# Optimization experiments

Measured on AMD Instinct MI355X. Metric: run time of the kernel, lower is better.

The kernel has to match this reference:

```python
import jax, jax.numpy as jnp
import numpy as np

NEG_INF = -jnp.inf


def _forward(q, k, v, q_indexer, k_indexer, weights, index_topk, end_pos):
    b, h, s, d = q.shape
    scale = float(1.0 / np.sqrt(d))

    # ---- bf16_index: per-head relu(qk) weighted-sum over indexer heads ----
    qi = jnp.swapaxes(q_indexer, 1, 2).astype(jnp.float32)        # [b,hi,s,di]
    ki = jnp.transpose(k_indexer, (0, 2, 3, 1)).astype(jnp.float32)  # [b,hk,di,s] (hk=1 broadcasts)
    p = jax.nn.relu(jnp.matmul(qi, ki))                            # [b,hi,s,s]
    index_score = jnp.einsum('bhqk,bqh->bqk', p, weights.astype(jnp.float32))  # [b,s,s]

    # ---- causal additive mask (attn_mask=None path) ----
    causal = jnp.where(jnp.triu(jnp.ones((s, s), bool), 1), NEG_INF, 0.0).astype(jnp.float32)
    index_score = index_score + causal[None]

    # ---- top-k sparse index selection ----
    K = min(int(index_topk), int(end_pos))
    topk_score, topk_idx = jax.lax.top_k(index_score, K)           # [b,s,K]
    qpos = jnp.arange(s)[None, :, None]
    valid = topk_idx <= qpos
    # invalid slots: torch writes -1 (wraps to last col on CUDA); last col is causally
    # masked for those rows, so dropping the scatter gives an identical final mask.
    scatter_idx = jnp.where(valid, topk_idx, s)
    index_mask = jnp.full((b, s, s), NEG_INF).at[
        jnp.arange(b)[:, None, None], jnp.arange(s)[None, :, None], scatter_idx
    ].set(0.0, mode='drop')

    am = causal[None] + index_mask                                 # [b,s,s]
    masked = jnp.isinf(am) & (am < 0)                              # True = masked out
    keep = ~masked[:, None]                                        # [b,1,s,s]

    # ---- sparse SDPA ----
    scores = jnp.einsum('bhqd,bhkd->bhqk', q, k) * scale
    scores = jnp.where(keep, scores, NEG_INF)
    attn = jax.nn.softmax(scores.astype(jnp.float32), axis=-1)     # [b,h,s,s]
    output = jnp.einsum('bhqk,bhkd->bhqd', attn.astype(q.dtype), v)

    # ---- indexer auxiliary loss (main attn dist uses detached q,k) ----
    main_attn_dist = jax.lax.stop_gradient(attn).sum(axis=1)       # [b,s,s]
    gather_idx = jnp.where(valid, topk_idx, s - 1)                 # -1 wraps to last col
    sel = jnp.take_along_axis(main_attn_dist, gather_idx, axis=-1) # [b,s,K]
    pdist = jax.nn.softmax(topk_score.astype(jnp.float32), axis=-1)
    tgt = sel / jnp.maximum(jnp.sum(jnp.abs(sel), axis=-1, keepdims=True), 1e-12)
    # F.kl_div(log(p+eps), tgt+eps): t*(log t - log p)
    kl = (tgt + 1e-8) * (jnp.log(tgt + 1e-8) - jnp.log(pdist + 1e-8))
    loss = kl.sum(-1).mean()
    return loss, output


def setup_inputs() -> dict:
    key = jax.random.key(0)
    ks = jax.random.split(key, 6)
    b, h, s, d = 1, 16, 2048, 128
    hi, di = 16, 128
    return {
        'q': jax.random.normal(ks[0], (b, h, s, d), jnp.float32),
        'k': jax.random.normal(ks[1], (b, h, s, d), jnp.float32),
        'v': jax.random.normal(ks[2], (b, h, s, d), jnp.float32),
        'q_indexer': jax.random.normal(ks[3], (b, s, hi, di), jnp.float32),
        'k_indexer': jax.random.normal(ks[4], (b, s, 1, di), jnp.float32),
        'weights': jax.random.uniform(ks[5], (b, s, hi), jnp.float32),
        'index_topk': 512,
        'end_pos': 2048,
    }


def reference(q, k, v, q_indexer, k_indexer, weights, index_topk, end_pos):
    return _forward(q, k, v, q_indexer, k_indexer, weights, index_topk, end_pos)
```

## Files before the change

### kernel.cpp

```cpp
#include <hip/hip_runtime.h>
#include <hip/hip_bf16.h>
#include <hip/hip_fp16.h>
#include <math.h>

#define S    2048
#define HQ   16
#define D    128
#define HI   16
#define DI   128
#define KSEL 512
#define OPW  132

typedef __attribute__((ext_vector_type(8))) short short8;
typedef __attribute__((ext_vector_type(4))) float f32x4;
typedef __attribute__((ext_vector_type(2))) float f32x2;
typedef __attribute__((ext_vector_type(2))) _Float16 h2v;

__device__ __forceinline__ float waveReduceSum(float v) {
#pragma unroll
    for (int o = 32; o > 0; o >>= 1) v += __shfl_down(v, o);
    return v;
}
__device__ __forceinline__ float waveReduceMax(float v) {
#pragma unroll
    for (int o = 32; o > 0; o >>= 1) v = fmaxf(v, __shfl_down(v, o));
    return v;
}
__device__ __forceinline__ float blockReduceSum(float v, float* tmp) {
    int wid = threadIdx.x >> 6, lane = threadIdx.x & 63;
    v = waveReduceSum(v);
    __syncthreads();
    if (lane == 0) tmp[wid] = v;
    __syncthreads();
    return tmp[0] + tmp[1] + tmp[2] + tmp[3];
}
__device__ __forceinline__ float blockReduceMax(float v, float* tmp) {
    int wid = threadIdx.x >> 6, lane = threadIdx.x & 63;
    v = waveReduceMax(v);
    __syncthreads();
    if (lane == 0) tmp[wid] = v;
    __syncthreads();
    return fmaxf(fmaxf(tmp[0], tmp[1]), fmaxf(tmp[2], tmp[3]));
}

__device__ __forceinline__ unsigned short f2bf(float f) {
    unsigned int u = __float_as_uint(f);
    return (unsigned short)((u + 0x7FFFu + ((u >> 16) & 1u)) >> 16);
}
__device__ __forceinline__ float bf2f(unsigned short h) {
    return __uint_as_float(((unsigned int)h) << 16);
}
__device__ __forceinline__ float fdot2u(unsigned int a, unsigned int b, float c) {
    return __builtin_amdgcn_fdot2(__builtin_bit_cast(h2v, a),
                                  __builtin_bit_cast(h2v, b), c, false);
}
__device__ __forceinline__ f32x2 f2shfl_xor(f32x2 v, int m) {
    f32x2 r;
    r.x = __shfl_xor(v.x, m);
    r.y = __shfl_xor(v.y, m);
    return r;
}

__global__ __launch_bounds__(256) void convert_kv(const float* __restrict__ kin,
                                                  const float* __restrict__ vin,
                                                  unsigned short* __restrict__ Kh,
                                                  unsigned int* __restrict__ Vq,
                                                  int n4) {
    const int stride = gridDim.x * 256;
    for (int i = blockIdx.x * 256 + threadIdx.x; i < n4; i += stride) {
        float4 x = ((const float4*)kin)[i];
        uint2 r;
        r.x = __builtin_bit_cast(unsigned int, __floats2half2_rn(x.x, x.y));
        r.y = __builtin_bit_cast(unsigned int, __floats2half2_rn(x.z, x.w));
        ((uint2*)Kh)[i] = r;
        float4 y = ((const float4*)vin)[i];
        int u = 0;
        u = __builtin_amdgcn_cvt_pk_fp8_f32(y.x, y.y, u, false);
        u = __builtin_amdgcn_cvt_pk_fp8_f32(y.z, y.w, u, true);
        Vq[i] = (unsigned int)u;
    }
}

__device__ __forceinline__ void split4(const float* in, unsigned short* hi,
                                       unsigned short* lo, int i) {
    float4 x = ((const float4*)in)[i];
    ushort4 h4, l4;
    h4.x = f2bf(x.x); l4.x = f2bf(x.x - bf2f(h4.x));
    h4.y = f2bf(x.y); l4.y = f2bf(x.y - bf2f(h4.y));
    h4.z = f2bf(x.z); l4.z = f2bf(x.z - bf2f(h4.z));
    h4.w = f2bf(x.w); l4.w = f2bf(x.w - bf2f(h4.w));
    ((ushort4*)hi)[i] = h4;
    ((ushort4*)lo)[i] = l4;
}
__global__ __launch_bounds__(256) void split_qiki(
    const float* __restrict__ qi, unsigned short* __restrict__ qih,
    unsigned short* __restrict__ qil,
    const float* __restrict__ ki, unsigned short* __restrict__ kih,
    unsigned short* __restrict__ kil, int n4q, int n4k) {
    const int stride = gridDim.x * 256;
    for (int i = blockIdx.x * 256 + threadIdx.x; i < n4q; i += stride)
        split4(qi, qih, qil, i);
    for (int i = blockIdx.x * 256 + threadIdx.x; i < n4k; i += stride)
        split4(ki, kih, kil, i);
}

__device__ void topk_from_scores(const float* scores, int ncand, int K, int q,
                                 int* __restrict__ topk_idx, float* __restrict__ topk_score,
                                 unsigned int* bins, unsigned int* sh_u, unsigned int* cnt_p) {
    const int tid = threadIdx.x;
    if (ncand <= K) {
        for (int j = tid; j < KSEL; j += 256) {
            if (j < ncand) {
                topk_idx[q * KSEL + j]   = j;
                topk_score[q * KSEL + j] = scores[j];
            } else {
                topk_idx[q * KSEL + j]   = -1;
                topk_score[q * KSEL + j] = -INFINITY;
            }
        }
        __syncthreads();
        return;
    }

    unsigned int prefix = 0;
    int need = K;
    for (int pass = 0; pass < 4; ++pass) {
        const int shift = 24 - pass * 8;
        for (int b = tid; b < 256; b += 256) bins[b] = 0;
        __syncthreads();
        const unsigned int himask = (pass == 0) ? 0u : (0xFFFFFFFFu << (shift + 8));
        for (int k = tid; k < ncand; k += 256) {
            unsigned int u = __float_as_uint(scores[k]);
            if ((u & himask) == prefix) atomicAdd(&bins[(u >> shift) & 0xFF], 1u);
        }
        __syncthreads();
        if (tid < 64) {
            const int l = tid;
            unsigned int b0 = bins[4 * l], b1 = bins[4 * l + 1],
                         b2 = bins[4 * l + 2], b3 = bins[4 * l + 3];
            unsigned int s3 = b3, s2 = b2 + s3, s1 = b1 + s2, s0 = b0 + s1;
            unsigned int acc = s0;
#pragma unroll
            for (int off = 1; off < 64; off <<= 1) {
                unsigned int t = __shfl_down(acc, off);
                if (l + off < 64) acc += t;
            }
            const unsigned int above = acc - s0;
            const unsigned int S0 = s0 + above, S1 = s1 + above,
                               S2 = s2 + above, S3 = s3 + above;
            const unsigned int nd = (unsigned int)need;
            if (4 * l + 0 >= 1 && S0 >= nd && S1 < nd) {
                sh_u[0] = prefix | ((unsigned int)(4 * l + 0) << shift);
                sh_u[1] = nd - S1;
            }
            if (S1 >= nd && S2 < nd) {
                sh_u[0] = prefix | ((unsigned int)(4 * l + 1) << shift);
                sh_u[1] = nd - S2;
            }
            if (S2 >= nd && S3 < nd) {
                sh_u[0] = prefix | ((unsigned int)(4 * l + 2) << shift);
                sh_u[1] = nd - S3;
            }
            if (S3 >= nd && above < nd) {
                sh_u[0] = prefix | ((unsigned int)(4 * l + 3) << shift);
                sh_u[1] = nd - above;
            }
            if (l == 0 && S1 < nd) {
                sh_u[0] = prefix;
                sh_u[1] = nd - S1;
            }
        }
        __syncthreads();
        prefix = sh_u[0];
        need   = (int)sh_u[1];
        __syncthreads();
    }
    const unsigned int ueqT = prefix;
    const int count_eq = (int)bins[ueqT & 0xFF];
    __syncthreads();
    if (tid == 0) *cnt_p = 0;
    __syncthreads();

    for (int k = tid; k < ncand; k += 256) {
        unsigned int u = __float_as_uint(scores[k]);
        if (u > ueqT) {
            unsigned int slot = atomicAdd(cnt_p, 1u);
            topk_idx[q * KSEL + slot]   = k;
            topk_score[q * KSEL + slot] = scores[k];
        }
    }
    __syncthreads();
    if (count_eq == need) {
        for (int k = tid; k < ncand; k += 256) {
            if (__float_as_uint(scores[k]) == ueqT) {
                unsigned int slot = atomicAdd(cnt_p, 1u);
                topk_idx[q * KSEL + slot]   = k;
                topk_score[q * KSEL + slot] = __uint_as_float(ueqT);
            }
        }
    } else if (tid == 0) {
        int emitted = 0;
        for (int k = 0; k < ncand && emitted < need; ++k) {
            if (__float_as_uint(scores[k]) == ueqT) {
                unsigned int slot = atomicAdd(cnt_p, 1u);
                topk_idx[q * KSEL + slot]   = k;
                topk_score[q * KSEL + slot] = __uint_as_float(ueqT);
                emitted++;
            }
        }
    }
    __syncthreads();
}

__global__ __launch_bounds__(256) void indexer_mfma(
    const unsigned short* __restrict__ qih, const unsigned short* __restrict__ qil,
    const unsigned short* __restrict__ kih, const unsigned short* __restrict__ kil,
    const float* __restrict__ w,
    const int* __restrict__ topk_p, const int* __restrict__ endpos_p,
    int* __restrict__ topk_idx, float* __restrict__ topk_score)
{
    const int tid  = threadIdx.x;
    const int wv   = tid >> 6;
    const int lane = tid & 63;
    int K = min(topk_p[0], endpos_p[0]);
    K = min(K, KSEL);

    __shared__ float scores[S];
    __shared__ float w_sh[HI];
    __shared__ unsigned int bins[256];
    __shared__ unsigned int sh_u[3];
    __shared__ unsigned int cnt;

    const int mrow = lane & 15;
    const int kgrp = lane >> 4;

    const int b = blockIdx.x;
    for (int qq = 0; qq < 2; ++qq) {
        const int q = qq ? (S - 1 - b) : b;
        if (tid < HI) w_sh[tid] = w[q * HI + tid];
        __syncthreads();

        short8 Ah[4], Al[4];
        {
            const unsigned short* bh = qih + ((size_t)q * HI + mrow) * DI + kgrp * 8;
            const unsigned short* bl = qil + ((size_t)q * HI + mrow) * DI + kgrp * 8;
#pragma unroll
            for (int dc = 0; dc < 4; dc++) {
                Ah[dc] = *(const short8*)(bh + dc * 32);
                Al[dc] = *(const short8*)(bl + dc * 32);
            }
        }
        float wreg[4];
#pragma unroll
        for (int e = 0; e < 4; e++) wreg[e] = w_sh[4 * kgrp + e];

        const int nkt = (q >> 4) + 1;
        for (int t = wv; t < nkt; t += 4) {
            const int k0 = t * 16;
            const unsigned short* bh = kih + ((size_t)(k0 + mrow)) * DI + kgrp * 8;
            const unsigned short* bl = kil + ((size_t)(k0 + mrow)) * DI + kgrp * 8;
            f32x4 acc = {0.f, 0.f, 0.f, 0.f};
#pragma unroll
            for (int dc = 0; dc < 4; dc++) {
                short8 Bh = *(const short8*)(bh + dc * 32);
                short8 Bl = *(const short8*)(bl + dc * 32);
                acc = __builtin_amdgcn_mfma_f32_16x16x32_bf16(Ah[dc], Bh, acc, 0, 0, 0);
                acc = __builtin_amdgcn_mfma_f32_16x16x32_bf16(Ah[dc], Bl, acc, 0, 0, 0);
                acc = __builtin_amdgcn_mfma_f32_16x16x32_bf16(Al[dc], Bh, acc, 0, 0, 0);
            }
            float part = wreg[0] * fmaxf(acc[0], 0.f) + wreg[1] * fmaxf(acc[1], 0.f)
                       + wreg[2] * fmaxf(acc[2], 0.f) + wreg[3] * fmaxf(acc[3], 0.f);
            part += __shfl_xor(part, 16);
            part += __shfl_xor(part, 32);
            if (lane < 16) {
                int k = k0 + lane;
                if (k <= q) scores[k] = part;
            }
        }
        __syncthreads();
        topk_from_scores(scores, q + 1, K, q, topk_idx, topk_score, bins, sh_u, &cnt);
    }
}

__global__ __launch_bounds__(256) void indexer_topk(
    const float* __restrict__ qi,
    const float* __restrict__ ki,
    const float* __restrict__ w,
    const int* __restrict__ topk_p, const int* __restrict__ endpos_p,
    int* __restrict__ topk_idx,
    float* __restrict__ topk_score)
{
    const int q   = blockIdx.x;
    const int tid = threadIdx.x;
    int K = min(topk_p[0], endpos_p[0]);
    K = min(K, KSEL);

    __shared__ float qis[HI * DI];
    __shared__ float wsh[HI];
    __shared__ float scores[S];
    __shared__ unsigned int bins[256];
    __shared__ unsigned int sh_u[3];
    __shared__ unsigned int cnt;

    for (int i = tid; i < HI * DI; i += 256) qis[i] = qi[(size_t)q * HI * DI + i];
    if (tid < HI) wsh[tid] = w[q * HI + tid];
    __syncthreads();

    const int ncand = q + 1;

    for (int kbase = 0; kbase < ncand; kbase += 1024) {
        const int k0 = kbase + tid * 4;
        if (k0 < ncand) {
            float acc[4][HI];
#pragma unroll
            for (int a = 0; a < 4; a++)
#pragma unroll
                for (int h = 0; h < HI; h++) acc[a][h] = 0.f;
            for (int d0 = 0; d0 < DI; d0 += 4) {
                float4 kv[4];
#pragma unroll
                for (int a = 0; a < 4; a++)
                    kv[a] = *(const float4*)&ki[(size_t)(k0 + a) * DI + d0];
#pragma unroll
                for (int h = 0; h < HI; h++) {
                    float4 qv = *(const float4*)&qis[h * DI + d0];
#pragma unroll
                    for (int a = 0; a < 4; a++) {
                        acc[a][h] += qv.x * kv[a].x + qv.y * kv[a].y +
                                     qv.z * kv[a].z + qv.w * kv[a].w;
                    }
                }
            }
#pragma unroll
            for (int a = 0; a < 4; a++) {
                int k = k0 + a;
                if (k < ncand) {
                    float s = 0.f;
#pragma unroll
                    for (int h = 0; h < HI; h++) s += wsh[h] * fmaxf(acc[a][h], 0.f);
                    scores[k] = s;
                }
            }
        }
    }
    __syncthreads();
    topk_from_scores(scores, ncand, K, q, topk_idx, topk_score, bins, sh_u, &cnt);
}

__global__ __launch_bounds__(256) void sparse_attn_v8(
    const float* __restrict__ Q,
    const unsigned short* __restrict__ Kh,
    const unsigned char* __restrict__ Vq,
    const int* __restrict__ topk_idx,
    const int* __restrict__ topk_p, const int* __restrict__ endpos_p,
    float* __restrict__ out,
    float* __restrict__ aacc_g)
{
    const int q   = blockIdx.x;
    const int h   = blockIdx.y;
    const int tid = threadIdx.x;
    int K = min(topk_p[0], endpos_p[0]);
    K = min(K, KSEL);
    const int n = min(q + 1, K);
    const float scale = 0.08838834764831845f;

    __shared__ int          offs[KSEL];
    __shared__ float        sc[KSEL];
    __shared__ unsigned int qh_u[64];
    __shared__ float        opart[16][OPW];
    __shared__ float        tmp[4];

    if (tid < 32) {
        float4 f = ((const float4*)&Q[((size_t)h * S + q) * D])[tid];
        qh_u[2 * tid]     = __builtin_bit_cast(unsigned int,
                              __floats2half2_rn(f.x * scale, f.y * scale));
        qh_u[2 * tid + 1] = __builtin_bit_cast(unsigned int,
                              __floats2half2_rn(f.z * scale, f.w * scale));
    }
    for (int j = tid; j < n; j += 256) offs[j] = topk_idx[q * KSEL + j] << 8;
    __syncthreads();

    const int l8 = tid & 7, grp8 = tid >> 3;
    unsigned int qa[4], qb[4];
#pragma unroll
    for (int c = 0; c < 4; c++) {
        qa[c] = qh_u[l8 * 4 + c];
        qb[c] = qh_u[32 + l8 * 4 + c];
    }
    const char* kbase = (const char*)Kh + (size_t)h * S * 256;
    const char* vbase = (const char*)Vq + (size_t)h * S * 128;

    float lsum = 0.f;
    f32x2 o2[8];
#pragma unroll
    for (int i = 0; i < 8; i++) o2[i] = (f32x2){0.f, 0.f};
    for (int j = grp8; j < n; j += 32) {
        const int off = offs[j];
        const char* rb = kbase + off;
        uint4 ra   = *(const uint4*)(rb + l8 * 16);
        uint4 rb2  = *(const uint4*)(rb + 128 + l8 * 16);
        uint4 vraw = *(const uint4*)(vbase + (off >> 1) + l8 * 16);
        float acc0 = fdot2u(ra.x, qa[0], 0.f);
        float acc1 = fdot2u(rb2.x, qb[0], 0.f);
        acc0 = fdot2u(ra.y, qa[1], acc0);
        acc1 = fdot2u(rb2.y, qb[1], acc1);
        acc0 = fdot2u(ra.z, qa[2], acc0);
        acc1 = fdot2u(rb2.z, qb[2], acc1);
        acc0 = fdot2u(ra.w, qa[3], acc0);
        acc1 = fdot2u(rb2.w, qb[3], acc1);
        float acc = acc0 + acc1;
        acc += __shfl_xor(acc, 1);
        acc += __shfl_xor(acc, 2);
        acc += __shfl_xor(acc, 4);
        const float p = __expf(acc);
        if (l8 == 0) sc[j] = p;
        lsum += p;
        const f32x2 p2 = {p, p};
        o2[0] += p2 * __builtin_amdgcn_cvt_pk_f32_fp8((int)vraw.x, false);
        o2[1] += p2 * __builtin_amdgcn_cvt_pk_f32_fp8((int)vraw.x, true);
        o2[2] += p2 * __builtin_amdgcn_cvt_pk_f32_fp8((int)vraw.y, false);
        o2[3] += p2 * __builtin_amdgcn_cvt_pk_f32_fp8((int)vraw.y, true);
        o2[4] += p2 * __builtin_amdgcn_cvt_pk_f32_fp8((int)vraw.z, false);
        o2[5] += p2 * __builtin_amdgcn_cvt_pk_f32_fp8((int)vraw.z, true);
        o2[6] += p2 * __builtin_amdgcn_cvt_pk_f32_fp8((int)vraw.w, false);
        o2[7] += p2 * __builtin_amdgcn_cvt_pk_f32_fp8((int)vraw.w, true);
    }
    lsum = blockReduceSum(lsum, tmp) * 0.125f;
    const float inv = 1.f / lsum;

    for (int j = tid; j < n; j += 256)
        atomicAdd(&aacc_g[(size_t)q * KSEL + j], sc[j] * inv);

#pragma unroll
    for (int i = 0; i < 8; i++) o2[i] += f2shfl_xor(o2[i], 32);
    const int lane = tid & 63, wvi = tid >> 6;
    if (lane < 32) {
        const int row = wvi * 4 + (lane >> 3);
        float* dst = &opart[row][(lane & 7) * 16];
#pragma unroll
        for (int i = 0; i < 8; i += 2) {
            float4 s;
            s.x = o2[i].x;     s.y = o2[i].y;
            s.z = o2[i + 1].x; s.w = o2[i + 1].y;
            *(float4*)&dst[i * 2] = s;
        }
    }
    __syncthreads();
    if (tid < D) {
        float s = 0.f;
#pragma unroll
        for (int p16 = 0; p16 < 16; ++p16) s += opart[p16][tid];
        out[((size_t)h * S + q) * D + tid] = s * inv;
    }
}

__global__ __launch_bounds__(256) void sparse_attn2(
    const float* __restrict__ Q,
    const float* __restrict__ Km,
    const float* __restrict__ V,
    const int* __restrict__ topk_idx,
    const int* __restrict__ topk_p, const int* __restrict__ endpos_p,
    float* __restrict__ out,
    float* __restrict__ aacc_g)
{
    const int q   = blockIdx.x;
    const int h   = blockIdx.y;
    const int tid = threadIdx.x;
    int K = min(topk_p[0], endpos_p[0]);
    K = min(K, KSEL);
    const int n = min(q + 1, K);
    const float scale = 0.08838834764831845f;

    __shared__ float qvec[D];
    __shared__ int   idxs[KSEL];
    __shared__ float sc[KSEL];
    __shared__ float opart[8][D];
    __shared__ float tmp[4];

    if (tid < 32)
        *(float4*)&qvec[tid * 4] = *(const float4*)&Q[((size_t)h * S + q) * D + tid * 4];
    for (int j = tid; j < n; j += 256) idxs[j] = topk_idx[q * KSEL + j];
    __syncthreads();

    const int l16 = tid & 15, grp = tid >> 4;
    const float4 q1 = *(const float4*)&qvec[l16 * 4];
    const float4 q2 = *(const float4*)&qvec[64 + l16 * 4];
    float lmax = -INFINITY;
    for (int j = grp; j < n; j += 16) {
        const float* kr = &Km[((size_t)h * S + idxs[j]) * D];
        float4 k1 = *(const float4*)&kr[l16 * 4];
        float4 k2 = *(const float4*)&kr[64 + l16 * 4];
        float acc = q1.x * k1.x + q1.y * k1.y + q1.z * k1.z + q1.w * k1.w
                  + q2.x * k2.x + q2.y * k2.y + q2.z * k2.z + q2.w * k2.w;
        acc += __shfl_xor(acc, 1);
        acc += __shfl_xor(acc, 2);
        acc += __shfl_xor(acc, 4);
        acc += __shfl_xor(acc, 8);
        float s = acc * scale;
        if (l16 == 0) sc[j] = s;
        lmax = fmaxf(lmax, s);
    }
    const float m = blockReduceMax(lmax, tmp);

    float lsum = 0.f;
    for (int j = tid; j < n; j += 256) {
        float p = expf(sc[j] - m);
        sc[j] = p;
        lsum += p;
    }
    lsum = blockReduceSum(lsum, tmp);
    const float inv = 1.f / lsum;
    for (int j = tid; j < n; j += 256) {
        float p = sc[j] * inv;
        sc[j] = p;
        atomicAdd(&aacc_g[(size_t)q * KSEL + j], p);
    }
    __syncthreads();

    const int jg = tid >> 5, lD = (tid & 31) * 4;
    float4 o4 = make_float4(0.f, 0.f, 0.f, 0.f);
    for (int j = jg; j < n; j += 8) {
        const float p = sc[j];
        float4 vv = *(const float4*)&V[((size_t)h * S + idxs[j]) * D + lD];
        o4.x += p * vv.x; o4.y += p * vv.y; o4.z += p * vv.z; o4.w += p * vv.w;
    }
    *(float4*)&opart[jg][lD] = o4;
    __syncthreads();
    if (tid < D) {
        float o = 0.f;
#pragma unroll
        for (int p8 = 0; p8 < 8; ++p8) o += opart[p8][tid];
        out[((size_t)h * S + q) * D + tid] = o;
    }
}

__global__ __launch_bounds__(256) void row_loss(
    const float* __restrict__ aacc_g,
    const float* __restrict__ topk_score,
    const int* __restrict__ topk_p, const int* __restrict__ endpos_p,
    float* __restrict__ rowloss)
{
    const int q   = blockIdx.x;
    const int tid = threadIdx.x;
    int K = min(topk_p[0], endpos_p[0]);
    K = min(K, KSEL);
    const int n = min(q + 1, K);

    __shared__ float sc[KSEL];
    __shared__ float aacc[KSEL];
    __shared__ float tmp[4];

    for (int j = tid; j < n; j += 256) aacc[j] = aacc_g[(size_t)q * KSEL + j];

    float tmaxl = -INFINITY;
    for (int j = tid; j < n; j += 256) {
        float t = topk_score[q * KSEL + j];
        sc[j] = t;
        tmaxl = fmaxf(tmaxl, t);
    }
    const float tm = blockReduceMax(tmaxl, tmp);
    float tsum = 0.f;
    for (int j = tid; j < n; j += 256) {
        float e = __expf(sc[j] - tm);
        sc[j] = e;
        tsum += e;
    }
    tsum = blockReduceSum(tsum, tmp);
    const float tinv = 1.f / tsum;

    float sa = 0.f;
    for (int j = tid; j < n; j += 256) sa += fabsf(aacc[j]);
    sa = blockReduceSum(sa, tmp);
    const float denom = fmaxf(sa, 1e-12f);

    float kl = 0.f;
    for (int j = tid; j < n; j += 256) {
        float tgt = aacc[j] / denom + 1e-8f;
        float pd  = sc[j] * tinv + 1e-8f;
        kl += tgt * (__logf(tgt) - __logf(pd));
    }
    kl = blockReduceSum(kl, tmp);
    if (tid == 0) rowloss[q] = kl;
}

__global__ __launch_bounds__(256) void reduce_loss(const float* __restrict__ rowloss,
                                                   float* __restrict__ out) {
    __shared__ float tmp[4];
    float v = 0.f;
    for (int i = threadIdx.x; i < S; i += 256) v += rowloss[i];
    v = blockReduceSum(v, tmp);
    if (threadIdx.x == 0) out[0] = v / (float)S;
}

extern "C" void kernel_launch(void* const* d_in, const int* in_sizes, int n_in,
                              void* d_out, int out_size, void* d_ws, size_t ws_size,
                              hipStream_t stream) {
    const float* q   = (const float*)d_in[0];
    const float* k   = (const float*)d_in[1];
    const float* v   = (const float*)d_in[2];
    const float* qi  = (const float*)d_in[3];
    const float* ki  = (const float*)d_in[4];
    const float* w   = (const float*)d_in[5];
    const int* topk  = (const int*)d_in[6];
    const int* endp  = (const int*)d_in[7];
    float* out = (float*)d_out;

    char* ws = (char*)d_ws;
    const size_t MB = 1ull << 20;
    int*   topk_idx   = (int*)ws;
    float* topk_score = (float*)(ws + 4 * MB);
    float* aacc_g     = (float*)(ws + 8 * MB);
    float* rowloss    = (float*)(ws + 12 * MB);
    char*  pbuf       = ws + 12 * MB + 65536;
    unsigned short* Kh  = (unsigned short*)pbuf;
    unsigned char*  Vq  = (unsigned char*)(pbuf + 8 * MB);
    unsigned short* qih = (unsigned short*)(pbuf + 12 * MB);
    unsigned short* qil = (unsigned short*)(pbuf + 20 * MB);
    unsigned short* kih = (unsigned short*)(pbuf + 28 * MB);
    unsigned short* kil = (unsigned short*)(pbuf + 28 * MB + 512 * 1024);
    const size_t need_attn = 12 * MB + 65536 + 12 * MB;
    const size_t need_idx  = 12 * MB + 65536 + 29 * MB;

    if (ws_size >= need_idx) {
        hipLaunchKernelGGL(split_qiki, dim3(2048), dim3(256), 0, stream,
                           qi, qih, qil, ki, kih, kil,
                           S * HI * DI / 4, S * DI / 4);
        hipLaunchKernelGGL(indexer_mfma, dim3(S / 2), dim3(256), 0, stream,
                           qih, qil, kih, kil, w, topk, endp, topk_idx, topk_score);
    } else {
        hipLaunchKernelGGL(indexer_topk, dim3(S), dim3(256), 0, stream,
                           qi, ki, w, topk, endp, topk_idx, topk_score);
    }

    hipMemsetAsync(aacc_g, 0, (size_t)S * KSEL * sizeof(float), stream);

    if (ws_size >= need_attn) {
        const int n4 = HQ * S * D / 4;
        hipLaunchKernelGGL(convert_kv, dim3(2048), dim3(256), 0, stream,
                           k, v, Kh, (unsigned int*)Vq, n4);
        hipLaunchKernelGGL(sparse_attn_v8, dim3(S, HQ), dim3(256), 0, stream,
                           q, Kh, Vq, topk_idx, topk, endp, out + 1, aacc_g);
    } else {
        hipLaunchKernelGGL(sparse_attn2, dim3(S, HQ), dim3(256), 0, stream,
                           q, k, v, topk_idx, topk, endp, out + 1, aacc_g);
    }

    hipLaunchKernelGGL(row_loss, dim3(S), dim3(256), 0, stream,
                       aacc_g, topk_score, topk, endp, rowloss);
    hipLaunchKernelGGL(reduce_loss, dim3(1), dim3(256), 0, stream,
                       rowloss, out);
}
```

Before: 374.5 us.

## Fuse preprocessing kernels and widen per-thread key rows in sparse attention

Merges the KV conversion, indexer hi/lo split, and accumulator memset into one prep kernel, cutting two launches and a memset from the sequence. The sparse attention kernel now gives each selected key row to 4 threads instead of 8, so each thread loads 64 bytes of K and 32 bytes of V and needs one fewer shuffle step in the dot-product reduction. In exchange each thread holds more registers (16 query words, 32 output accumulators), which may lower occupancy, and the output cross-lane reduction gains an extra shuffle stage.

```diff
diff --git a/kernel.cpp b/kernel.cpp
--- a/kernel.cpp
+++ b/kernel.cpp
@@ -60,14 +60,30 @@
     r.y = __shfl_xor(v.y, m);
     return r;
 }
-
-__global__ __launch_bounds__(256) void convert_kv(const float* __restrict__ kin,
-                                                  const float* __restrict__ vin,
-                                                  unsigned short* __restrict__ Kh,
-                                                  unsigned int* __restrict__ Vq,
-                                                  int n4) {
+__device__ __forceinline__ void split4(const float* in, unsigned short* hi,
+                                       unsigned short* lo, int i) {
+    float4 x = ((const float4*)in)[i];
+    ushort4 h4, l4;
+    h4.x = f2bf(x.x); l4.x = f2bf(x.x - bf2f(h4.x));
+    h4.y = f2bf(x.y); l4.y = f2bf(x.y - bf2f(h4.y));
+    h4.z = f2bf(x.z); l4.z = f2bf(x.z - bf2f(h4.z));
+    h4.w = f2bf(x.w); l4.w = f2bf(x.w - bf2f(h4.w));
+    ((ushort4*)hi)[i] = h4;
+    ((ushort4*)lo)[i] = l4;
+}
+
+__global__ __launch_bounds__(256) void prep_all(
+    const float* __restrict__ kin, const float* __restrict__ vin,
+    unsigned short* __restrict__ Kh, unsigned int* __restrict__ Vq,
+    const float* __restrict__ qi, unsigned short* __restrict__ qih,
+    unsigned short* __restrict__ qil,
+    const float* __restrict__ ki, unsigned short* __restrict__ kih,
+    unsigned short* __restrict__ kil,
+    float* __restrict__ aacc_g,
+    int n4kv, int n4q, int n4k, int n4acc) {
     const int stride = gridDim.x * 256;
-    for (int i = blockIdx.x * 256 + threadIdx.x; i < n4; i += stride) {
+    const int t0 = blockIdx.x * 256 + threadIdx.x;
+    for (int i = t0; i < n4kv; i += stride) {
         float4 x = ((const float4*)kin)[i];
         uint2 r;
         r.x = __builtin_bit_cast(unsigned int, __floats2half2_rn(x.x, x.y));
@@ -79,29 +95,10 @@
         u = __builtin_amdgcn_cvt_pk_fp8_f32(y.z, y.w, u, true);
         Vq[i] = (unsigned int)u;
     }
-}
-
-__device__ __forceinline__ void split4(const float* in, unsigned short* hi,
-                                       unsigned short* lo, int i) {
-    float4 x = ((const float4*)in)[i];
-    ushort4 h4, l4;
-    h4.x = f2bf(x.x); l4.x = f2bf(x.x - bf2f(h4.x));
-    h4.y = f2bf(x.y); l4.y = f2bf(x.y - bf2f(h4.y));
-    h4.z = f2bf(x.z); l4.z = f2bf(x.z - bf2f(h4.z));
-    h4.w = f2bf(x.w); l4.w = f2bf(x.w - bf2f(h4.w));
-    ((ushort4*)hi)[i] = h4;
-    ((ushort4*)lo)[i] = l4;
-}
-__global__ __launch_bounds__(256) void split_qiki(
-    const float* __restrict__ qi, unsigned short* __restrict__ qih,
-    unsigned short* __restrict__ qil,
-    const float* __restrict__ ki, unsigned short* __restrict__ kih,
-    unsigned short* __restrict__ kil, int n4q, int n4k) {
-    const int stride = gridDim.x * 256;
-    for (int i = blockIdx.x * 256 + threadIdx.x; i < n4q; i += stride)
-        split4(qi, qih, qil, i);
-    for (int i = blockIdx.x * 256 + threadIdx.x; i < n4k; i += stride)
-        split4(ki, kih, kil, i);
+    for (int i = t0; i < n4q; i += stride) split4(qi, qih, qil, i);
+    for (int i = t0; i < n4k; i += stride) split4(ki, kih, kil, i);
+    float4 z = make_float4(0.f, 0.f, 0.f, 0.f);
+    for (int i = t0; i < n4acc; i += stride) ((float4*)aacc_g)[i] = z;
 }
 
 __device__ void topk_from_scores(const float* scores, int ncand, int K, int q,
@@ -347,7 +344,7 @@
     topk_from_scores(scores, ncand, K, q, topk_idx, topk_score, bins, sh_u, &cnt);
 }
 
-__global__ __launch_bounds__(256) void sparse_attn_v8(
+__global__ __launch_bounds__(256) void sparse_attn_v9(
     const float* __restrict__ Q,
     const unsigned short* __restrict__ Kh,
     const unsigned char* __restrict__ Vq,
@@ -380,65 +377,76 @@
     for (int j = tid; j < n; j += 256) offs[j] = topk_idx[q * KSEL + j] << 8;
     __syncthreads();
 
-    const int l8 = tid & 7, grp8 = tid >> 3;
-    unsigned int qa[4], qb[4];
-#pragma unroll
-    for (int c = 0; c < 4; c++) {
-        qa[c] = qh_u[l8 * 4 + c];
-        qb[c] = qh_u[32 + l8 * 4 + c];
-    }
+    const int l4 = tid & 3, grp = tid >> 2;
+    unsigned int qreg[16];
+#pragma unroll
+    for (int c = 0; c < 16; c++) qreg[c] = qh_u[l4 * 16 + c];
     const char* kbase = (const char*)Kh + (size_t)h * S * 256;
     const char* vbase = (const char*)Vq + (size_t)h * S * 128;
 
     float lsum = 0.f;
-    f32x2 o2[8];
-#pragma unroll
-    for (int i = 0; i < 8; i++) o2[i] = (f32x2){0.f, 0.f};
-    for (int j = grp8; j < n; j += 32) {
+    f32x2 o2[16];
+#pragma unroll
+    for (int i = 0; i < 16; i++) o2[i] = (f32x2){0.f, 0.f};
+    for (int j = grp; j < n; j += 64) {
         const int off = offs[j];
-        const char* rb = kbase + off;
-        uint4 ra   = *(const uint4*)(rb + l8 * 16);
-        uint4 rb2  = *(const uint4*)(rb + 128 + l8 * 16);
-        uint4 vraw = *(const uint4*)(vbase + (off >> 1) + l8 * 16);
-        float acc0 = fdot2u(ra.x, qa[0], 0.f);
-        float acc1 = fdot2u(rb2.x, qb[0], 0.f);
-        acc0 = fdot2u(ra.y, qa[1], acc0);
-        acc1 = fdot2u(rb2.y, qb[1], acc1);
-        acc0 = fdot2u(ra.z, qa[2], acc0);
-        acc1 = fdot2u(rb2.z, qb[2], acc1);
-        acc0 = fdot2u(ra.w, qa[3], acc0);
-        acc1 = fdot2u(rb2.w, qb[3], acc1);
+        const char* rb = kbase + off + l4 * 64;
+        uint4 ka = *(const uint4*)(rb);
+        uint4 kb = *(const uint4*)(rb + 16);
+        uint4 kc = *(const uint4*)(rb + 32);
+        uint4 kd = *(const uint4*)(rb + 48);
+        const char* vb = vbase + (off >> 1) + l4 * 32;
+        uint4 va  = *(const uint4*)(vb);
+        uint4 vb2 = *(const uint4*)(vb + 16);
+        float acc0 = fdot2u(ka.x, qreg[0], 0.f);
+        float acc1 = fdot2u(kc.x, qreg[8], 0.f);
+        acc0 = fdot2u(ka.y, qreg[1], acc0);  acc1 = fdot2u(kc.y, qreg[9],  acc1);
+        acc0 = fdot2u(ka.z, qreg[2], acc0);  acc1 = fdot2u(kc.z, qreg[10], acc1);
+        acc0 = fdot2u(ka.w, qreg[3], acc0);  acc1 = fdot2u(kc.w, qreg[11], acc1);
+        acc0 = fdot2u(kb.x, qreg[4], acc0);  acc1 = fdot2u(kd.x, qreg[12], acc1);
+        acc0 = fdot2u(kb.y, qreg[5], acc0);  acc1 = fdot2u(kd.y, qreg[13], acc1);
+        acc0 = fdot2u(kb.z, qreg[6], acc0);  acc1 = fdot2u(kd.z, qreg[14], acc1);
+        acc0 = fdot2u(kb.w, qreg[7], acc0);  acc1 = fdot2u(kd.w, qreg[15], acc1);
         float acc = acc0 + acc1;
         acc += __shfl_xor(acc, 1);
         acc += __shfl_xor(acc, 2);
-        acc += __shfl_xor(acc, 4);
         const float p = __expf(acc);
-        if (l8 == 0) sc[j] = p;
+        if (l4 == 0) sc[j] = p;
         lsum += p;
         const f32x2 p2 = {p, p};
-        o2[0] += p2 * __builtin_amdgcn_cvt_pk_f32_fp8((int)vraw.x, false);
-        o2[1] += p2 * __builtin_amdgcn_cvt_pk_f32_fp8((int)vraw.x, true);
-        o2[2] += p2 * __builtin_amdgcn_cvt_pk_f32_fp8((int)vraw.y, false);
-        o2[3] += p2 * __builtin_amdgcn_cvt_pk_f32_fp8((int)vraw.y, true);
-        o2[4] += p2 * __builtin_amdgcn_cvt_pk_f32_fp8((int)vraw.z, false);
-        o2[5] += p2 * __builtin_amdgcn_cvt_pk_f32_fp8((int)vraw.z, true);
-        o2[6] += p2 * __builtin_amdgcn_cvt_pk_f32_fp8((int)vraw.w, false);
-        o2[7] += p2 * __builtin_amdgcn_cvt_pk_f32_fp8((int)vraw.w, true);
-    }
-    lsum = blockReduceSum(lsum, tmp) * 0.125f;
+        o2[0]  += p2 * __builtin_amdgcn_cvt_pk_f32_fp8((int)va.x,  false);
+        o2[1]  += p2 * __builtin_amdgcn_cvt_pk_f32_fp8((int)va.x,  true);
+        o2[2]  += p2 * __builtin_amdgcn_cvt_pk_f32_fp8((int)va.y,  false);
+        o2[3]  += p2 * __builtin_amdgcn_cvt_pk_f32_fp8((int)va.y,  true);
+        o2[4]  += p2 * __builtin_amdgcn_cvt_pk_f32_fp8((int)va.z,  false);
+        o2[5]  += p2 * __builtin_amdgcn_cvt_pk_f32_fp8((int)va.z,  true);
+        o2[6]  += p2 * __builtin_amdgcn_cvt_pk_f32_fp8((int)va.w,  false);
+        o2[7]  += p2 * __builtin_amdgcn_cvt_pk_f32_fp8((int)va.w,  true);
+        o2[8]  += p2 * __builtin_amdgcn_cvt_pk_f32_fp8((int)vb2.x, false);
+        o2[9]  += p2 * __builtin_amdgcn_cvt_pk_f32_fp8((int)vb2.x, true);
+        o2[10] += p2 * __builtin_amdgcn_cvt_pk_f32_fp8((int)vb2.y, false);
+        o2[11] += p2 * __builtin_amdgcn_cvt_pk_f32_fp8((int)vb2.y, true);
+        o2[12] += p2 * __builtin_amdgcn_cvt_pk_f32_fp8((int)vb2.z, false);
+        o2[13] += p2 * __builtin_amdgcn_cvt_pk_f32_fp8((int)vb2.z, true);
+        o2[14] += p2 * __builtin_amdgcn_cvt_pk_f32_fp8((int)vb2.w, false);
+        o2[15] += p2 * __builtin_amdgcn_cvt_pk_f32_fp8((int)vb2.w, true);
+    }
+    lsum = blockReduceSum(lsum, tmp) * 0.25f;
     const float inv = 1.f / lsum;
 
     for (int j = tid; j < n; j += 256)
         atomicAdd(&aacc_g[(size_t)q * KSEL + j], sc[j] * inv);
 
 #pragma unroll
-    for (int i = 0; i < 8; i++) o2[i] += f2shfl_xor(o2[i], 32);
+    for (int i = 0; i < 16; i++) o2[i] += f2shfl_xor(o2[i], 32);
+#pragma unroll
+    for (int i = 0; i < 16; i++) o2[i] += f2shfl_xor(o2[i], 16);
     const int lane = tid & 63, wvi = tid >> 6;
-    if (lane < 32) {
-        const int row = wvi * 4 + (lane >> 3);
-        float* dst = &opart[row][(lane & 7) * 16];
-#pragma unroll
-        for (int i = 0; i < 8; i += 2) {
+    if (lane < 16) {
+        const int row = wvi * 4 + (lane >> 2);
+        float* dst = &opart[row][(lane & 3) * 32];
+#pragma unroll
+        for (int i = 0; i < 16; i += 2) {
             float4 s;
             s.x = o2[i].x;     s.y = o2[i].y;
             s.z = o2[i + 1].x; s.w = o2[i + 1].y;
@@ -621,26 +629,20 @@
     const size_t need_attn = 12 * MB + 65536 + 12 * MB;
     const size_t need_idx  = 12 * MB + 65536 + 29 * MB;
 
-    if (ws_size >= need_idx) {
-        hipLaunchKernelGGL(split_qiki, dim3(2048), dim3(256), 0, stream,
-                           qi, qih, qil, ki, kih, kil,
-                           S * HI * DI / 4, S * DI / 4);
+    if (ws_size >= need_idx && ws_size >= need_attn) {
+        hipLaunchKernelGGL(prep_all, dim3(2048), dim3(256), 0, stream,
+                           k, v, Kh, (unsigned int*)Vq,
+                           qi, qih, qil, ki, kih, kil, aacc_g,
+                           HQ * S * D / 4, S * HI * DI / 4, S * DI / 4,
+                           S * KSEL / 4);
         hipLaunchKernelGGL(indexer_mfma, dim3(S / 2), dim3(256), 0, stream,
                            qih, qil, kih, kil, w, topk, endp, topk_idx, topk_score);
+        hipLaunchKernelGGL(sparse_attn_v9, dim3(S, HQ), dim3(256), 0, stream,
+                           q, Kh, Vq, topk_idx, topk, endp, out + 1, aacc_g);
     } else {
         hipLaunchKernelGGL(indexer_topk, dim3(S), dim3(256), 0, stream,
                            qi, ki, w, topk, endp, topk_idx, topk_score);
-    }
-
-    hipMemsetAsync(aacc_g, 0, (size_t)S * KSEL * sizeof(float), stream);
-
-    if (ws_size >= need_attn) {
-        const int n4 = HQ * S * D / 4;
-        hipLaunchKernelGGL(convert_kv, dim3(2048), dim3(256), 0, stream,
-                           k, v, Kh, (unsigned int*)Vq, n4);
-        hipLaunchKernelGGL(sparse_attn_v8, dim3(S, HQ), dim3(256), 0, stream,
-                           q, Kh, Vq, topk_idx, topk, endp, out + 1, aacc_g);
-    } else {
+        hipMemsetAsync(aacc_g, 0, (size_t)S * KSEL * sizeof(float), stream);
         hipLaunchKernelGGL(sparse_attn2, dim3(S, HQ), dim3(256), 0, stream,
                            q, k, v, topk_idx, topk, endp, out + 1, aacc_g);
     }
```

New measurement: 455.8 us. +21.7%, slower.
